# Kernel optimization log

Measured on AMD Instinct MI355X. Metric: run time of the kernel, lower is better.

## Reference

```python
import jax, jax.numpy as jnp
import numpy as np

B, IN, OUT, ORDER = 8192, 1024, 1024, 7


def setup_inputs() -> dict:
    key = jax.random.key(0)
    k1, k2 = jax.random.split(key)
    x = jax.random.normal(k1, (B, IN), dtype=jnp.float32)
    tanh_range = jnp.float32(1.0)
    coef = jax.random.normal(k2, (OUT, IN, ORDER + 1), dtype=jnp.float32) * 0.1
    return {"x": x, "tanh_range": tanh_range, "coef": coef}


def _poly(x, tanh_range, order):
    # t^0, t^1, ..., t^order via cumulative products (matches torch recurrence)
    t = jnp.tanh(x * tanh_range)                      # [B, IN]
    powers = jnp.cumprod(jnp.broadcast_to(t[..., None], t.shape + (order,)), axis=-1)
    ones = jnp.ones_like(t)[..., None]
    return jnp.concatenate([ones, powers], axis=-1)   # [B, IN, order+1]


def reference(x, tanh_range, coef):
    poly = _poly(x, tanh_range, ORDER)                # [B, IN, K]
    # output[b, j] = sum_{i,k} coef[j,i,k] * poly[b,i,k]
    return jnp.einsum('bik,jik->bj', poly, coef)
```

## Files before the change

### kernel.cpp

```cpp
#include <hip/hip_runtime.h>
#include <hip/hip_bf16.h>


#define BM 128
#define BN 128
#define BK 64
#define KDIM 8192

typedef short bf16x8 __attribute__((ext_vector_type(8)));
typedef short bf16x4 __attribute__((ext_vector_type(4)));
typedef float f32x4  __attribute__((ext_vector_type(4)));

__device__ __forceinline__ unsigned short f2bf(float f) {
    union { float f; unsigned u; } v; v.f = f;
    unsigned r = v.u + 0x7fffu + ((v.u >> 16) & 1u);
    return (unsigned short)(r >> 16);
}

__device__ __forceinline__ void gload_lds16(const void* gp, void* lp) {
    __builtin_amdgcn_global_load_lds(
        (const __attribute__((address_space(1))) void*)gp,
        (__attribute__((address_space(3))) void*)lp, 16, 0, 0);
}

#define COEF_BLOCKS 8192
#define TANH_BLOCKS 32768

__global__ __launch_bounds__(256)
void prep(const float* __restrict__ x, const float* __restrict__ trp,
          const float4* __restrict__ coef, bf16x4* __restrict__ coef_bf,
          bf16x8* __restrict__ A) {
    const int b = blockIdx.x;
    if (b < COEF_BLOCKS) {
        const int i = b * 256 + threadIdx.x;
        const float4 v = coef[i];
        bf16x4 p;
        p[0] = (short)f2bf(v.x); p[1] = (short)f2bf(v.y);
        p[2] = (short)f2bf(v.z); p[3] = (short)f2bf(v.w);
        coef_bf[i] = p;
    } else {
        const int i = (b - COEF_BLOCKS) * 256 + threadIdx.x;
        const float tr = trp[0];
        const float xv = x[i];
        const float e  = __expf(2.0f * tr * xv);
        const float tt = 1.0f - 2.0f * __builtin_amdgcn_rcpf(e + 1.0f);
        bf16x8 pk;
        float p = 1.0f;
        #pragma unroll
        for (int k = 0; k < 8; ++k) { pk[k] = (short)f2bf(p); p *= tt; }
        A[i] = pk;
    }
}

__global__ __launch_bounds__(256, 2)
void gemm_bt(const unsigned short* __restrict__ A, const unsigned short* __restrict__ Bt,
             float* __restrict__ out)
{
    __shared__ unsigned short As[BM * BK];
    __shared__ unsigned short Bs[BN * BK];

    const int t    = threadIdx.x;
    const int m0   = blockIdx.x * BM;
    const int n0   = blockIdx.y * BN;
    const int w    = t >> 6;
    const int lane = t & 63;
    const int wm   = (w >> 1) * 64;
    const int wn   = (w & 1) * 64;
    const int lrow = lane & 15;

    const int srow   = t >> 3;
    const int schunk = (t & 7) ^ (srow & 7);
    const int wbase  = w * 512;

    f32x4 acc[4][4];
    #pragma unroll
    for (int i = 0; i < 4; i++)
        #pragma unroll
        for (int j = 0; j < 4; j++)
            acc[i][j] = (f32x4){0.f, 0.f, 0.f, 0.f};

    const size_t abase = (size_t)(m0 + srow) * KDIM + schunk * 8;
    const size_t bbase = (size_t)(n0 + srow) * KDIM + schunk * 8;

    for (int k0 = 0; k0 < KDIM; k0 += BK) {
        #pragma unroll
        for (int r = 0; r < 4; ++r)
            gload_lds16(A + abase + (size_t)r * 32 * KDIM + k0, &As[r * 2048 + wbase]);
        #pragma unroll
        for (int r = 0; r < 4; ++r)
            gload_lds16(Bt + bbase + (size_t)r * 32 * KDIM + k0, &Bs[r * 2048 + wbase]);

        __syncthreads();

        #pragma unroll
        for (int kk = 0; kk < BK; kk += 32) {
            const int soff = ((((kk >> 3) + (lane >> 4)) ^ (lane & 7)) * 8);
            bf16x8 a[4], b[4];
            #pragma unroll
            for (int i = 0; i < 4; i++)
                a[i] = *(const bf16x8*)&As[(wm + i * 16 + lrow) * BK + soff];
            #pragma unroll
            for (int j = 0; j < 4; j++)
                b[j] = *(const bf16x8*)&Bs[(wn + j * 16 + lrow) * BK + soff];
            #pragma unroll
            for (int i = 0; i < 4; i++)
                #pragma unroll
                for (int j = 0; j < 4; j++)
                    acc[i][j] = __builtin_amdgcn_mfma_f32_16x16x32_bf16(a[i], b[j], acc[i][j], 0, 0, 0);
        }

        __syncthreads();
    }

    const int crow = (lane >> 4) * 4;
    const int ccol = lane & 15;
    #pragma unroll
    for (int i = 0; i < 4; i++) {
        #pragma unroll
        for (int j = 0; j < 4; j++) {
            const int m = m0 + wm + i * 16 + crow;
            const int n = n0 + wn + j * 16 + ccol;
            #pragma unroll
            for (int r = 0; r < 4; ++r)
                out[(size_t)(m + r) * 1024 + n] = acc[i][j][r];
        }
    }
}

#define LDK 72
__global__ __launch_bounds__(256, 2)
void taylor_gemm(const float* __restrict__ x, const float* __restrict__ trp,
                 const float* __restrict__ coef, float* __restrict__ out)
{
    __shared__ unsigned short As[BM * LDK];
    __shared__ unsigned short Bs[BN * LDK];

    const int t  = threadIdx.x;
    const int m0 = blockIdx.x * BM;
    const int n0 = blockIdx.y * BN;
    const float tr = trp[0];

    const int w    = t >> 6;
    const int lane = t & 63;
    const int wm   = (w >> 1) * 64;
    const int wn   = (w & 1) * 64;
    const int lrow = lane & 15;
    const int kq   = (lane >> 4) * 8;

    f32x4 acc[4][4];
    #pragma unroll
    for (int i = 0; i < 4; i++)
        #pragma unroll
        for (int j = 0; j < 4; j++)
            acc[i][j] = (f32x4){0.f, 0.f, 0.f, 0.f};

    const int bcol  = t & 15;
    const int brow0 = t >> 4;
    const int acol  = t & 7;
    const int arow0 = t >> 3;

    for (int k0 = 0; k0 < KDIM; k0 += BK) {
        const int i0 = k0 >> 3;
        #pragma unroll
        for (int r = 0; r < 8; ++r) {
            const int row = brow0 + r * 16;
            const float4 v = *(const float4*)(coef + (size_t)(n0 + row) * KDIM + k0 + bcol * 4);
            bf16x4 pk;
            pk[0] = (short)f2bf(v.x); pk[1] = (short)f2bf(v.y);
            pk[2] = (short)f2bf(v.z); pk[3] = (short)f2bf(v.w);
            *(bf16x4*)&Bs[row * LDK + bcol * 4] = pk;
        }
        #pragma unroll
        for (int r = 0; r < 4; ++r) {
            const int row = arow0 + r * 32;
            const float xv = x[(size_t)(m0 + row) * 1024 + i0 + acol];
            const float e  = __expf(2.0f * tr * xv);
            const float tt = 1.0f - 2.0f / (e + 1.0f);
            bf16x8 pk;
            float p = 1.0f;
            #pragma unroll
            for (int k = 0; k < 8; ++k) { pk[k] = (short)f2bf(p); p *= tt; }
            *(bf16x8*)&As[row * LDK + acol * 8] = pk;
        }
        __syncthreads();
        #pragma unroll
        for (int kk = 0; kk < BK; kk += 32) {
            bf16x8 a[4], b[4];
            #pragma unroll
            for (int i = 0; i < 4; i++)
                a[i] = *(const bf16x8*)&As[(wm + i * 16 + lrow) * LDK + kk + kq];
            #pragma unroll
            for (int j = 0; j < 4; j++)
                b[j] = *(const bf16x8*)&Bs[(wn + j * 16 + lrow) * LDK + kk + kq];
            #pragma unroll
            for (int i = 0; i < 4; i++)
                #pragma unroll
                for (int j = 0; j < 4; j++)
                    acc[i][j] = __builtin_amdgcn_mfma_f32_16x16x32_bf16(a[i], b[j], acc[i][j], 0, 0, 0);
        }
        __syncthreads();
    }

    const int crow = (lane >> 4) * 4;
    const int ccol = lane & 15;
    #pragma unroll
    for (int i = 0; i < 4; i++) {
        #pragma unroll
        for (int j = 0; j < 4; j++) {
            const int m = m0 + wm + i * 16 + crow;
            const int n = n0 + wn + j * 16 + ccol;
            #pragma unroll
            for (int r = 0; r < 4; ++r)
                out[(size_t)(m + r) * 1024 + n] = acc[i][j][r];
        }
    }
}

extern "C" void kernel_launch(void* const* d_in, const int* in_sizes, int n_in,
                              void* d_out, int out_size, void* d_ws, size_t ws_size,
                              hipStream_t stream) {
    const float* x    = (const float*)d_in[0];
    const float* trp  = (const float*)d_in[1];
    const float* coef = (const float*)d_in[2];
    float* out = (float*)d_out;

    const size_t COEF_BYTES = (size_t)1024 * KDIM * 2;
    const size_t A_BYTES    = (size_t)8192 * KDIM * 2;
    dim3 block(256);

    if (ws_size >= COEF_BYTES + A_BYTES) {
        unsigned short* coef_bf = (unsigned short*)d_ws;
        unsigned short* A_bf    = (unsigned short*)((char*)d_ws + COEF_BYTES);

        prep<<<dim3(COEF_BLOCKS + TANH_BLOCKS), block, 0, stream>>>(
            x, trp, (const float4*)coef, (bf16x4*)coef_bf, (bf16x8*)A_bf);
        gemm_bt<<<dim3(8192 / BM, 1024 / BN), block, 0, stream>>>(
            A_bf, coef_bf, out);
    } else {
        taylor_gemm<<<dim3(8192 / BM, 1024 / BN), block, 0, stream>>>(x, trp, coef, out);
    }
}
```

Before: 248.1 us.

## Drop constant power term from GEMM K dimension and add it as per-column bias

The t^0 power column is always one, so its contribution is just a per-output sum of coef[:, :, 0]. That sum is now computed in a small bias kernel and added in the GEMM epilogue. K shrinks from 8192 to 7168, which cuts MFMA work and the bf16 workspace traffic by an eighth. The prep kernel is rewritten so each thread handles 8 inputs (64 coefficients) and emits packed 56-element rows, and the extra launch adds a little overhead.

```diff
diff --git a/kernel.cpp b/kernel.cpp
--- a/kernel.cpp
+++ b/kernel.cpp
@@ -5,7 +5,8 @@
 #define BM 128
 #define BN 128
 #define BK 64
-#define KDIM 8192
+#define KT 7168
+#define KFULL 8192
 
 typedef short bf16x8 __attribute__((ext_vector_type(8)));
 typedef short bf16x4 __attribute__((ext_vector_type(4)));
@@ -23,38 +24,79 @@
         (__attribute__((address_space(3))) void*)lp, 16, 0, 0);
 }
 
-#define COEF_BLOCKS 8192
-#define TANH_BLOCKS 32768
+#define CVT_BLOCKS  512
+#define TANH_BLOCKS 4096
 
 __global__ __launch_bounds__(256)
 void prep(const float* __restrict__ x, const float* __restrict__ trp,
-          const float4* __restrict__ coef, bf16x4* __restrict__ coef_bf,
-          bf16x8* __restrict__ A) {
+          const float* __restrict__ coef, unsigned short* __restrict__ coef_bf,
+          unsigned short* __restrict__ A) {
     const int b = blockIdx.x;
-    if (b < COEF_BLOCKS) {
-        const int i = b * 256 + threadIdx.x;
-        const float4 v = coef[i];
-        bf16x4 p;
-        p[0] = (short)f2bf(v.x); p[1] = (short)f2bf(v.y);
-        p[2] = (short)f2bf(v.z); p[3] = (short)f2bf(v.w);
-        coef_bf[i] = p;
+    unsigned short tmp[56];
+    if (b < CVT_BLOCKS) {
+        const size_t g = (size_t)b * 256 + threadIdx.x;
+        const float* src = coef + g * 64;
+        float buf[64];
+        #pragma unroll
+        for (int v = 0; v < 16; ++v) {
+            const float4 f = *(const float4*)(src + v * 4);
+            buf[v*4+0] = f.x; buf[v*4+1] = f.y; buf[v*4+2] = f.z; buf[v*4+3] = f.w;
+        }
+        #pragma unroll
+        for (int p = 0; p < 8; ++p)
+            #pragma unroll
+            for (int k = 1; k < 8; ++k)
+                tmp[p * 7 + k - 1] = f2bf(buf[p * 8 + k]);
+        bf16x8* dst = (bf16x8*)(coef_bf + g * 56);
+        #pragma unroll
+        for (int v = 0; v < 7; ++v) {
+            bf16x8 pk;
+            #pragma unroll
+            for (int s = 0; s < 8; ++s) pk[s] = (short)tmp[v * 8 + s];
+            dst[v] = pk;
+        }
     } else {
-        const int i = (b - COEF_BLOCKS) * 256 + threadIdx.x;
+        const size_t g = (size_t)(b - CVT_BLOCKS) * 256 + threadIdx.x;
         const float tr = trp[0];
-        const float xv = x[i];
-        const float e  = __expf(2.0f * tr * xv);
-        const float tt = 1.0f - 2.0f * __builtin_amdgcn_rcpf(e + 1.0f);
-        bf16x8 pk;
-        float p = 1.0f;
-        #pragma unroll
-        for (int k = 0; k < 8; ++k) { pk[k] = (short)f2bf(p); p *= tt; }
-        A[i] = pk;
-    }
+        const float4 x0 = *(const float4*)(x + g * 8);
+        const float4 x1 = *(const float4*)(x + g * 8 + 4);
+        const float xs[8] = {x0.x, x0.y, x0.z, x0.w, x1.x, x1.y, x1.z, x1.w};
+        #pragma unroll
+        for (int p = 0; p < 8; ++p) {
+            const float e  = __expf(2.0f * tr * xs[p]);
+            const float tt = 1.0f - 2.0f * __builtin_amdgcn_rcpf(e + 1.0f);
+            float pw = tt;
+            #pragma unroll
+            for (int k = 1; k < 8; ++k) { tmp[p * 7 + k - 1] = f2bf(pw); pw *= tt; }
+        }
+        bf16x8* dst = (bf16x8*)(A + g * 56);
+        #pragma unroll
+        for (int v = 0; v < 7; ++v) {
+            bf16x8 pk;
+            #pragma unroll
+            for (int s = 0; s < 8; ++s) pk[s] = (short)tmp[v * 8 + s];
+            dst[v] = pk;
+        }
+    }
+}
+
+__global__ __launch_bounds__(256)
+void bias_k(const float* __restrict__ coef, float* __restrict__ bias) {
+    const int j = blockIdx.x;
+    float s = 0.f;
+    for (int ii = threadIdx.x; ii < 1024; ii += 256)
+        s += coef[(size_t)j * KFULL + (size_t)ii * 8];
+    #pragma unroll
+    for (int off = 32; off > 0; off >>= 1) s += __shfl_down(s, off, 64);
+    __shared__ float ls[4];
+    if ((threadIdx.x & 63) == 0) ls[threadIdx.x >> 6] = s;
+    __syncthreads();
+    if (threadIdx.x == 0) bias[j] = ls[0] + ls[1] + ls[2] + ls[3];
 }
 
 __global__ __launch_bounds__(256, 2)
 void gemm_bt(const unsigned short* __restrict__ A, const unsigned short* __restrict__ Bt,
-             float* __restrict__ out)
+             const float* __restrict__ bias, float* __restrict__ out)
 {
     __shared__ unsigned short As[BM * BK];
     __shared__ unsigned short Bs[BN * BK];
@@ -79,16 +121,16 @@
         for (int j = 0; j < 4; j++)
             acc[i][j] = (f32x4){0.f, 0.f, 0.f, 0.f};
 
-    const size_t abase = (size_t)(m0 + srow) * KDIM + schunk * 8;
-    const size_t bbase = (size_t)(n0 + srow) * KDIM + schunk * 8;
-
-    for (int k0 = 0; k0 < KDIM; k0 += BK) {
+    const size_t abase = (size_t)(m0 + srow) * KT + schunk * 8;
+    const size_t bbase = (size_t)(n0 + srow) * KT + schunk * 8;
+
+    for (int k0 = 0; k0 < KT; k0 += BK) {
         #pragma unroll
         for (int r = 0; r < 4; ++r)
-            gload_lds16(A + abase + (size_t)r * 32 * KDIM + k0, &As[r * 2048 + wbase]);
+            gload_lds16(A + abase + (size_t)r * 32 * KT + k0, &As[r * 2048 + wbase]);
         #pragma unroll
         for (int r = 0; r < 4; ++r)
-            gload_lds16(Bt + bbase + (size_t)r * 32 * KDIM + k0, &Bs[r * 2048 + wbase]);
+            gload_lds16(Bt + bbase + (size_t)r * 32 * KT + k0, &Bs[r * 2048 + wbase]);
 
         __syncthreads();
 
@@ -115,14 +157,15 @@
     const int crow = (lane >> 4) * 4;
     const int ccol = lane & 15;
     #pragma unroll
-    for (int i = 0; i < 4; i++) {
-        #pragma unroll
-        for (int j = 0; j < 4; j++) {
+    for (int j = 0; j < 4; j++) {
+        const int n = n0 + wn + j * 16 + ccol;
+        const float bv = bias[n];
+        #pragma unroll
+        for (int i = 0; i < 4; i++) {
             const int m = m0 + wm + i * 16 + crow;
-            const int n = n0 + wn + j * 16 + ccol;
             #pragma unroll
             for (int r = 0; r < 4; ++r)
-                out[(size_t)(m + r) * 1024 + n] = acc[i][j][r];
+                out[(size_t)(m + r) * 1024 + n] = acc[i][j][r] + bv;
         }
     }
 }
@@ -159,12 +202,12 @@
     const int acol  = t & 7;
     const int arow0 = t >> 3;
 
-    for (int k0 = 0; k0 < KDIM; k0 += BK) {
+    for (int k0 = 0; k0 < KFULL; k0 += BK) {
         const int i0 = k0 >> 3;
         #pragma unroll
         for (int r = 0; r < 8; ++r) {
             const int row = brow0 + r * 16;
-            const float4 v = *(const float4*)(coef + (size_t)(n0 + row) * KDIM + k0 + bcol * 4);
+            const float4 v = *(const float4*)(coef + (size_t)(n0 + row) * KFULL + k0 + bcol * 4);
             bf16x4 pk;
             pk[0] = (short)f2bf(v.x); pk[1] = (short)f2bf(v.y);
             pk[2] = (short)f2bf(v.z); pk[3] = (short)f2bf(v.w);
@@ -224,18 +267,21 @@
     const float* coef = (const float*)d_in[2];
     float* out = (float*)d_out;
 
-    const size_t COEF_BYTES = (size_t)1024 * KDIM * 2;
-    const size_t A_BYTES    = (size_t)8192 * KDIM * 2;
+    const size_t A_BYTES    = (size_t)8192 * KT * 2;
+    const size_t COEF_BYTES = (size_t)1024 * KT * 2;
+    const size_t BIAS_BYTES = 1024 * sizeof(float);
     dim3 block(256);
 
-    if (ws_size >= COEF_BYTES + A_BYTES) {
-        unsigned short* coef_bf = (unsigned short*)d_ws;
-        unsigned short* A_bf    = (unsigned short*)((char*)d_ws + COEF_BYTES);
-
-        prep<<<dim3(COEF_BLOCKS + TANH_BLOCKS), block, 0, stream>>>(
-            x, trp, (const float4*)coef, (bf16x4*)coef_bf, (bf16x8*)A_bf);
+    if (ws_size >= A_BYTES + COEF_BYTES + BIAS_BYTES) {
+        unsigned short* A_bf    = (unsigned short*)d_ws;
+        unsigned short* coef_bf = (unsigned short*)((char*)d_ws + A_BYTES);
+        float*          bias    = (float*)((char*)d_ws + A_BYTES + COEF_BYTES);
+
+        prep<<<dim3(CVT_BLOCKS + TANH_BLOCKS), block, 0, stream>>>(
+            x, trp, coef, coef_bf, A_bf);
+        bias_k<<<dim3(1024), block, 0, stream>>>(coef, bias);
         gemm_bt<<<dim3(8192 / BM, 1024 / BN), block, 0, stream>>>(
-            A_bf, coef_bf, out);
+            A_bf, coef_bf, bias, out);
     } else {
         taylor_gemm<<<dim3(8192 / BM, 1024 / BN), block, 0, stream>>>(x, trp, coef, out);
     }
```

Result: slower. 265.0 us (+6.8%).
